# Kernel tuning notes

Hardware: AMD Instinct MI355X
Metric: run time of the kernel (lower is better)

## Reference

```python
import jax, jax.numpy as jnp
import numpy as np

B, N, F_IN, H, FO = 4, 2048, 256, 4, 64


def setup_inputs() -> dict:
    key = jax.random.key(0)
    k1, k2, k3, k4, k5 = jax.random.split(key, 5)
    x = jax.random.normal(k1, (B, N, F_IN), dtype=jnp.float32)
    # random 0/1 adjacency with self-loops so every row of softmax is finite
    adj = jax.random.randint(k2, (N, N), 0, 2).astype(jnp.float32)
    adj = jnp.maximum(adj, jnp.eye(N, dtype=jnp.float32))
    # parameters (xavier-uniform style)
    lim_w = float(np.sqrt(6.0 / (F_IN + H * FO)))
    W = jax.random.uniform(k3, (F_IN, H * FO), minval=-lim_w, maxval=lim_w, dtype=jnp.float32)
    lim_a = float(np.sqrt(6.0 / (H + FO)))
    a_src = jax.random.uniform(k4, (H, FO), minval=-lim_a, maxval=lim_a, dtype=jnp.float32)
    a_dst = jax.random.uniform(k5, (H, FO), minval=-lim_a, maxval=lim_a, dtype=jnp.float32)
    return {"x": x, "adj": adj, "W": W, "a_src": a_src, "a_dst": a_dst}


def reference(x, adj, W, a_src, a_dst):
    # h: (B, N, H, FO)
    h = (x @ W).reshape(B, N, H, FO)
    attn_src = jnp.einsum("bnhf,hf->bnh", h, a_src)  # (B,N,H)
    attn_dst = jnp.einsum("bnhf,hf->bnh", h, a_dst)  # (B,N,H)
    # scores[b,i,j,h] = src[b,i,h] + dst[b,j,h]
    scores = attn_src[:, :, None, :] + attn_dst[:, None, :, :]
    scores = jax.nn.leaky_relu(scores, negative_slope=0.2)
    mask = (adj == 0)[None, :, :, None]  # (1,N,N,1)
    scores = jnp.where(mask, -jnp.inf, scores)
    attn = jax.nn.softmax(scores, axis=2)  # softmax over neighbors j
    # dropout is identity in eval mode / p=0
    out = jnp.einsum("bijh,bjhf->bihf", attn, h)  # (B,N,H,FO)
    return out.reshape(B, N, H * FO)  # concat=True
```

## Files before the change

### kernel.cpp

```cpp
#include <hip/hip_runtime.h>
#include <hip/hip_bf16.h>
#include <math.h>

#define B 4
#define N 2048
#define FIN 256
#define H 4
#define FO 64
#define M (B*N)
#define HF (H*FO)

typedef __attribute__((ext_vector_type(8))) short short8;
typedef __attribute__((ext_vector_type(4))) float float4v;
typedef __attribute__((ext_vector_type(4))) int int4v;

#if __has_builtin(__builtin_amdgcn_exp2f)
#define EXP2(x) __builtin_amdgcn_exp2f(x)
#else
#define EXP2(x) exp2f(x)
#endif

static __device__ __forceinline__ unsigned int pk_rne(float a, float b) {
  unsigned int ua = __builtin_bit_cast(unsigned int, a);
  unsigned int ub = __builtin_bit_cast(unsigned int, b);
  ua += 0x7fffu + ((ua >> 16) & 1u);
  ub += 0x7fffu + ((ub >> 16) & 1u);
  return (ua >> 16) | (ub & 0xffff0000u);
}

static __device__ __forceinline__ unsigned int pk_trunc(float a, float b) {
#if __has_builtin(__builtin_amdgcn_perm)
  return __builtin_amdgcn_perm(__builtin_bit_cast(unsigned int, b),
                               __builtin_bit_cast(unsigned int, a), 0x07060302u);
#else
  return (__builtin_bit_cast(unsigned int, a) >> 16) |
         (__builtin_bit_cast(unsigned int, b) & 0xffff0000u);
#endif
}

static __device__ __forceinline__ void split_pair(float x0, float x1,
                                                  unsigned int& hi, unsigned int& lo) {
  unsigned int u0 = __builtin_bit_cast(unsigned int, x0);
  unsigned int u1 = __builtin_bit_cast(unsigned int, x1);
  hi = (u0 >> 16) | (u1 & 0xffff0000u);
  float h0 = __builtin_bit_cast(float, u0 & 0xffff0000u);
  float h1 = __builtin_bit_cast(float, u1 & 0xffff0000u);
  unsigned int l0 = __builtin_bit_cast(unsigned int, x0 - h0);
  unsigned int l1 = __builtin_bit_cast(unsigned int, x1 - h1);
  lo = (l0 >> 16) | (l1 & 0xffff0000u);
}

static __device__ __forceinline__ unsigned int fenc(float f) {
  unsigned int b = __builtin_bit_cast(unsigned int, f);
  return (b & 0x80000000u) ? ~b : (b | 0x80000000u);
}
static __device__ __forceinline__ float fdec(unsigned int e) {
  unsigned int b = (e & 0x80000000u) ? (e & 0x7fffffffu) : ~e;
  return __builtin_bit_cast(float, b);
}

__global__ __launch_bounds__(256) void prep_wx(const float* __restrict__ Wsrc,
                                               const float* __restrict__ X,
                                               unsigned short* __restrict__ Wf_hi,
                                               unsigned short* __restrict__ Wf_lo,
                                               unsigned short* __restrict__ Xf_hi,
                                               unsigned short* __restrict__ Xf_lo,
                                               unsigned int* __restrict__ DmaxEnc) {
  const int blk = blockIdx.x;
  const int t = threadIdx.x;
  __shared__ float lds[64][65];
  if (blk < 16) {
    if (blk == 0 && t < 16) DmaxEnc[t] = 0u;
    const int k0 = (blk >> 2) * 64;
    const int h  = blk & 3;
    const int n0 = h * 64;
    const int c4 = (t & 15) * 4;
    #pragma unroll
    for (int rep = 0; rep < 4; ++rep) {
      const int kl = (t >> 4) + 16 * rep;
      const float4 v = *(const float4*)(Wsrc + (size_t)(k0 + kl) * HF + n0 + c4);
      lds[kl][c4 + 0] = v.x; lds[kl][c4 + 1] = v.y;
      lds[kl][c4 + 2] = v.z; lds[kl][c4 + 3] = v.w;
    }
    __syncthreads();
    #pragma unroll
    for (int rep = 0; rep < 2; ++rep) {
      const int s   = t + rep * 256;
      const int kcl = s >> 8;
      const int tt  = (s >> 6) & 3;
      const int ln  = s & 63;
      const int fL  = tt * 16 + (ln & 15);
      const int kb  = kcl * 32 + (ln >> 4) * 8;
      unsigned int hv[4], lv[4];
      #pragma unroll
      for (int p = 0; p < 4; ++p)
        split_pair(lds[kb + 2 * p][fL], lds[kb + 2 * p + 1][fL], hv[p], lv[p]);
      const size_t off = ((((size_t)h * 8 + (k0 >> 5) + kcl) * 4 + tt) << 9) + ln * 8;
      *(uint4*)(Wf_hi + off) = make_uint4(hv[0], hv[1], hv[2], hv[3]);
      *(uint4*)(Wf_lo + off) = make_uint4(lv[0], lv[1], lv[2], lv[3]);
    }
    return;
  }
  const int xblk  = blk - 16;
  const int mrow0 = xblk * 64;
  for (int ktile = 0; ktile < 4; ++ktile) {
    if (ktile) __syncthreads();
    const int k0 = ktile * 64;
    const int c4 = (t & 15) * 4;
    #pragma unroll
    for (int rep = 0; rep < 4; ++rep) {
      const int rl = (t >> 4) + 16 * rep;
      const float4 v = *(const float4*)(X + (size_t)(mrow0 + rl) * FIN + k0 + c4);
      lds[rl][c4 + 0] = v.x; lds[rl][c4 + 1] = v.y;
      lds[rl][c4 + 2] = v.z; lds[rl][c4 + 3] = v.w;
    }
    __syncthreads();
    #pragma unroll
    for (int rep = 0; rep < 2; ++rep) {
      const int s   = t + rep * 256;
      const int mt  = s >> 7;
      const int kcl = (s >> 6) & 1;
      const int ln  = s & 63;
      const int mrl = mt * 16 + (ln & 15);
      const int kb  = kcl * 32 + (ln >> 4) * 8;
      unsigned int hv[4], lv[4];
      #pragma unroll
      for (int p = 0; p < 4; ++p)
        split_pair(lds[mrl][kb + 2 * p], lds[mrl][kb + 2 * p + 1], hv[p], lv[p]);
      const size_t off = (((size_t)(xblk * 4 + mt) * 8 + (ktile * 2 + kcl)) << 9) + ln * 8;
      *(uint4*)(Xf_hi + off) = make_uint4(hv[0], hv[1], hv[2], hv[3]);
      *(uint4*)(Xf_lo + off) = make_uint4(lv[0], lv[1], lv[2], lv[3]);
    }
  }
}

__global__ __launch_bounds__(256) void gemm_fused(const unsigned short* __restrict__ Xf_hi,
                                                  const unsigned short* __restrict__ Xf_lo,
                                                  const unsigned short* __restrict__ Wf_hi,
                                                  const unsigned short* __restrict__ Wf_lo,
                                                  const float* __restrict__ adj,
                                                  const float* __restrict__ a_src,
                                                  const float* __restrict__ a_dst,
                                                  float* __restrict__ Srcv,
                                                  float2* __restrict__ Epair,
                                                  unsigned int* __restrict__ DmaxEnc,
                                                  unsigned long long* __restrict__ packed,
                                                  unsigned short* __restrict__ Hf) {
  if (blockIdx.x >= 512) {
    const int row = blockIdx.x - 512;
    const int pw = threadIdx.x >> 6, pl = threadIdx.x & 63;
    const float* ar = adj + (size_t)row * N;
    for (int c = pw; c < N / 64; c += 4) {
      unsigned long long m = __ballot(ar[c * 64 + pl] != 0.f);
      if (pl == 0) packed[(size_t)row * (N / 64) + c] = m;
    }
    return;
  }
  __shared__ unsigned short sh[64][72];
  __shared__ float smax[4];
  const int xcd  = blockIdx.x & 7;
  const int slot = blockIdx.x >> 3;
  const int mb = xcd * 16 + (slot >> 2);
  const int h  = slot & 3;
  const int w = threadIdx.x >> 6, lane = threadIdx.x & 63;
  const int fl = lane & 15, quad = lane >> 4;
  const float L2E = 1.4426950408889634f;

  const float4v zero = {0.f, 0.f, 0.f, 0.f};
  float4v acc[4] = {zero, zero, zero, zero};

  const size_t abase = (((size_t)(mb * 4 + w) * 8) << 9) + lane * 8;
  #pragma unroll
  for (int kc = 0; kc < 8; ++kc) {
    const short8 Ahi = *(const short8*)(Xf_hi + abase + ((size_t)kc << 9));
    const short8 Alo = *(const short8*)(Xf_lo + abase + ((size_t)kc << 9));
    #pragma unroll
    for (int t = 0; t < 4; ++t) {
      const size_t woff = ((((size_t)h * 8 + kc) * 4 + t) << 9) + lane * 8;
      const short8 Bhi = *(const short8*)(Wf_hi + woff);
      const short8 Blo = *(const short8*)(Wf_lo + woff);
      acc[t] = __builtin_amdgcn_mfma_f32_16x16x32_bf16(Ahi, Bhi, acc[t], 0, 0, 0);
      acc[t] = __builtin_amdgcn_mfma_f32_16x16x32_bf16(Alo, Bhi, acc[t], 0, 0, 0);
      acc[t] = __builtin_amdgcn_mfma_f32_16x16x32_bf16(Ahi, Blo, acc[t], 0, 0, 0);
    }
  }

  const int bb  = (mb * 64) >> 11;
  const int n0w = (mb * 64) & (N - 1);
  const int bh  = bb * H + h;
  float as[4], ad[4];
  #pragma unroll
  for (int t = 0; t < 4; ++t) {
    as[t] = a_src[h * FO + t * 16 + fl];
    ad[t] = a_dst[h * FO + t * 16 + fl];
  }
  float wmax = -INFINITY;
  #pragma unroll
  for (int reg = 0; reg < 4; ++reg) {
    float sv = 0.f, dv = 0.f;
    #pragma unroll
    for (int t = 0; t < 4; ++t) {
      sv = fmaf(acc[t][reg], as[t], sv);
      dv = fmaf(acc[t][reg], ad[t], dv);
    }
    #pragma unroll
    for (int off = 1; off <= 8; off <<= 1) {
      sv += __shfl_xor(sv, off, 64);
      dv += __shfl_xor(dv, off, 64);
    }
    wmax = fmaxf(wmax, dv);
    if (fl == 0) {
      const int node = n0w + w * 16 + quad * 4 + reg;
      Srcv[(bh << 11) + node] = sv;
      float2 e;
      e.x = EXP2(dv * L2E);
      e.y = EXP2(dv * (0.2f * L2E));
      Epair[(bh << 11) + node] = e;
    }
  }
  wmax = fmaxf(wmax, __shfl_xor(wmax, 16, 64));
  wmax = fmaxf(wmax, __shfl_xor(wmax, 32, 64));
  if (lane == 0) smax[w] = wmax;

  #pragma unroll
  for (int t = 0; t < 4; ++t) {
    const int nl = w * 16 + quad * 4;
    *(unsigned int*)&sh[t * 16 + fl][nl]     = pk_rne(acc[t][0], acc[t][1]);
    *(unsigned int*)&sh[t * 16 + fl][nl + 2] = pk_rne(acc[t][2], acc[t][3]);
  }
  __syncthreads();
  if (threadIdx.x == 0) {
    const float bmax = fmaxf(fmaxf(smax[0], smax[1]), fmaxf(smax[2], smax[3]));
    atomicMax(DmaxEnc + bh, fenc(bmax));
  }
  const int jc0 = n0w >> 5;
  #pragma unroll
  for (int rep = 0; rep < 2; ++rep) {
    const int s = (int)threadIdx.x + rep * 256;
    const int jcl = s >> 8;
    const int tt  = (s >> 6) & 3;
    const int ln  = s & 63;
    const int f    = tt * 16 + (ln & 15);
    const int node = jcl * 32 + (ln >> 4) * 8;
    unsigned short* dsth = Hf + (((size_t)bh * 64 + jc0 + jcl) * 4 + tt) * 512 + ln * 8;
    *(uint4*)dsth = *(const uint4*)&sh[f][node];
  }
}

__global__ __launch_bounds__(512) void gat_mfma(const unsigned char* __restrict__ pb,
                                                const float* __restrict__ Src,
                                                const float2* __restrict__ Epair,
                                                const unsigned int* __restrict__ DmaxEnc,
                                                const unsigned short* __restrict__ Hf,
                                                float* __restrict__ out) {
  const int xcd  = blockIdx.x & 7;
  const int slot = blockIdx.x >> 3;
  const int b    = xcd >> 1;
  const int i0   = ((xcd & 1) * 32 + slot) * 32;
  const int w    = threadIdx.x >> 6;
  const int lane = threadIdx.x & 63;
  const int h    = w & 3;
  const int jh   = w >> 2;
  const int bh   = b * H + h;
  const int fl   = lane & 15;
  const int kk   = (lane >> 4) * 8;
  const float L2E = 1.4426950408889634f;

  const int row0 = i0 + fl;
  const int row1 = i0 + 16 + fl;
  const float dmx = fdec(DmaxEnc[bh]);
  const float s0 = Src[(bh << 11) + row0];
  const float s1 = Src[(bh << 11) + row1];
  const float u0 = s0 + dmx, m0 = fmaxf(u0, 0.2f * u0);
  const float u1 = s1 + dmx, m1 = fmaxf(u1, 0.2f * u1);
  const float c1a = EXP2((s0 - m0) * L2E), c2a = EXP2((0.2f * s0 - m0) * L2E);
  const float c1b = EXP2((s1 - m1) * L2E), c2b = EXP2((0.2f * s1 - m1) * L2E);
  const float ta = EXP2(-s0 * L2E), tb = EXP2(-s1 * L2E);
  const float* ep = (const float*)(Epair + (bh << 11));
  const unsigned char* pb0 = pb + (size_t)row0 * (N / 8);
  const unsigned char* pb1 = pb + (size_t)row1 * (N / 8);
  const unsigned short* hfb = Hf + (size_t)bh * 64 * 2048 + lane * 8;

  const short onebf = 0x3F80;
  short8 ones;
  #pragma unroll
  for (int jj = 0; jj < 8; ++jj) ones[jj] = onebf;

  const float4v zero = {0.f, 0.f, 0.f, 0.f};
  float4v acc[2][4];
  float4v accL[2];
  #pragma unroll
  for (int rt = 0; rt < 2; ++rt) {
    accL[rt] = zero;
    #pragma unroll
    for (int t = 0; t < 4; ++t) acc[rt][t] = zero;
  }

  const int jbeg = jh * (N / 2);
  short8 nb0, nb1, nb2, nb3;
  float4 nq0, nq1, nq2, nq3;
  unsigned int nm0, nm1;
  {
    const unsigned short* hc = hfb + (size_t)(jbeg >> 5) * 2048;
    nb0 = *(const short8*)(hc + 0 * 512);
    nb1 = *(const short8*)(hc + 1 * 512);
    nb2 = *(const short8*)(hc + 2 * 512);
    nb3 = *(const short8*)(hc + 3 * 512);
    nq0 = *(const float4*)(ep + 2 * (jbeg + kk) + 0);
    nq1 = *(const float4*)(ep + 2 * (jbeg + kk) + 4);
    nq2 = *(const float4*)(ep + 2 * (jbeg + kk) + 8);
    nq3 = *(const float4*)(ep + 2 * (jbeg + kk) + 12);
    nm0 = pb0[(jbeg + kk) >> 3];
    nm1 = pb1[(jbeg + kk) >> 3];
  }

  for (int it = 0; it < 32; ++it) {
    const short8 b0 = nb0, b1 = nb1, b2 = nb2, b3 = nb3;
    const float4 q0 = nq0, q1 = nq1, q2 = nq2, q3 = nq3;
    const unsigned int mk0 = nm0, mk1 = nm1;
    if (it < 31) {
      const int jn = jbeg + (it + 1) * 32;
      const unsigned short* hc = hfb + (size_t)(jn >> 5) * 2048;
      nb0 = *(const short8*)(hc + 0 * 512);
      nb1 = *(const short8*)(hc + 1 * 512);
      nb2 = *(const short8*)(hc + 2 * 512);
      nb3 = *(const short8*)(hc + 3 * 512);
      nq0 = *(const float4*)(ep + 2 * (jn + kk) + 0);
      nq1 = *(const float4*)(ep + 2 * (jn + kk) + 4);
      nq2 = *(const float4*)(ep + 2 * (jn + kk) + 8);
      nq3 = *(const float4*)(ep + 2 * (jn + kk) + 12);
      nm0 = pb0[(jn + kk) >> 3];
      nm1 = pb1[(jn + kk) >> 3];
    }
    const float E1v[8] = {q0.x, q0.z, q1.x, q1.z, q2.x, q2.z, q3.x, q3.z};
    const float E2v[8] = {q0.y, q0.w, q1.y, q1.w, q2.y, q2.w, q3.y, q3.w};
    int p0i[4], p1i[4];
    #pragma unroll
    for (int p = 0; p < 4; ++p) {
      const int e0 = 2 * p, e1 = 2 * p + 1;
      const bool sa0 = E1v[e0] > ta;
      float va0 = (sa0 ? c1a : c2a) * (sa0 ? E1v[e0] : E2v[e0]);
      va0 = ((mk0 >> e0) & 1u) ? va0 : 0.f;
      const bool sa1 = E1v[e1] > ta;
      float va1 = (sa1 ? c1a : c2a) * (sa1 ? E1v[e1] : E2v[e1]);
      va1 = ((mk0 >> e1) & 1u) ? va1 : 0.f;
      p0i[p] = (int)pk_trunc(va0, va1);
      const bool sb0 = E1v[e0] > tb;
      float vb0 = (sb0 ? c1b : c2b) * (sb0 ? E1v[e0] : E2v[e0]);
      vb0 = ((mk1 >> e0) & 1u) ? vb0 : 0.f;
      const bool sb1 = E1v[e1] > tb;
      float vb1 = (sb1 ? c1b : c2b) * (sb1 ? E1v[e1] : E2v[e1]);
      vb1 = ((mk1 >> e1) & 1u) ? vb1 : 0.f;
      p1i[p] = (int)pk_trunc(vb0, vb1);
    }
    const short8 p0 = __builtin_bit_cast(short8, (int4v){p0i[0], p0i[1], p0i[2], p0i[3]});
    const short8 p1 = __builtin_bit_cast(short8, (int4v){p1i[0], p1i[1], p1i[2], p1i[3]});
    acc[0][0] = __builtin_amdgcn_mfma_f32_16x16x32_bf16(p0, b0, acc[0][0], 0, 0, 0);
    acc[0][1] = __builtin_amdgcn_mfma_f32_16x16x32_bf16(p0, b1, acc[0][1], 0, 0, 0);
    acc[0][2] = __builtin_amdgcn_mfma_f32_16x16x32_bf16(p0, b2, acc[0][2], 0, 0, 0);
    acc[0][3] = __builtin_amdgcn_mfma_f32_16x16x32_bf16(p0, b3, acc[0][3], 0, 0, 0);
    accL[0]   = __builtin_amdgcn_mfma_f32_16x16x32_bf16(p0, ones, accL[0], 0, 0, 0);
    acc[1][0] = __builtin_amdgcn_mfma_f32_16x16x32_bf16(p1, b0, acc[1][0], 0, 0, 0);
    acc[1][1] = __builtin_amdgcn_mfma_f32_16x16x32_bf16(p1, b1, acc[1][1], 0, 0, 0);
    acc[1][2] = __builtin_amdgcn_mfma_f32_16x16x32_bf16(p1, b2, acc[1][2], 0, 0, 0);
    acc[1][3] = __builtin_amdgcn_mfma_f32_16x16x32_bf16(p1, b3, acc[1][3], 0, 0, 0);
    accL[1]   = __builtin_amdgcn_mfma_f32_16x16x32_bf16(p1, ones, accL[1], 0, 0, 0);
  }

  __shared__ float4v parts[4][64][11];
  if (jh == 1) {
    #pragma unroll
    for (int rt = 0; rt < 2; ++rt) {
      #pragma unroll
      for (int t = 0; t < 4; ++t) parts[h][lane][rt * 5 + t] = acc[rt][t];
      parts[h][lane][rt * 5 + 4] = accL[rt];
    }
  }
  __syncthreads();
  if (jh == 0) {
    #pragma unroll
    for (int rt = 0; rt < 2; ++rt) {
      #pragma unroll
      for (int t = 0; t < 4; ++t) acc[rt][t] += parts[h][lane][rt * 5 + t];
      accL[rt] += parts[h][lane][rt * 5 + 4];
    }
    const int quad = lane >> 4;
    #pragma unroll
    for (int rt = 0; rt < 2; ++rt) {
      #pragma unroll
      for (int reg = 0; reg < 4; ++reg) {
        const int r = i0 + rt * 16 + quad * 4 + reg;
        const float invl = 1.f / accL[rt][reg];
        float* op = out + ((size_t)(b * N) + r) * HF + h * FO + fl;
        #pragma unroll
        for (int t = 0; t < 4; ++t) op[t * 16] = acc[rt][t][reg] * invl;
      }
    }
  }
}

extern "C" void kernel_launch(void* const* d_in, const int* in_sizes, int n_in,
                              void* d_out, int out_size, void* d_ws, size_t ws_size,
                              hipStream_t stream) {
  const float* x     = (const float*)d_in[0];
  const float* adj   = (const float*)d_in[1];
  const float* W     = (const float*)d_in[2];
  const float* a_src = (const float*)d_in[3];
  const float* a_dst = (const float*)d_in[4];
  float* out = (float*)d_out;

  char* p = (char*)d_ws;
  float* Srcv = (float*)p;                 p += (size_t)B * H * N * 4;
  float2* Epair = (float2*)p;              p += (size_t)B * H * N * 8;
  unsigned int* DmaxEnc = (unsigned int*)p; p += 256;
  unsigned short* Wfh = (unsigned short*)p; p += (size_t)HF * FIN * 2;
  unsigned short* Wfl = (unsigned short*)p; p += (size_t)HF * FIN * 2;
  unsigned short* Xfh = (unsigned short*)p; p += (size_t)M * FIN * 2;
  unsigned short* Xfl = (unsigned short*)p; p += (size_t)M * FIN * 2;
  unsigned short* Hf  = (unsigned short*)p; p += (size_t)M * HF * 2;
  unsigned long long* packed = (unsigned long long*)p;

  prep_wx<<<dim3(144), dim3(256), 0, stream>>>(W, x, Wfh, Wfl, Xfh, Xfl, DmaxEnc);
  gemm_fused<<<dim3(512 + N), dim3(256), 0, stream>>>(Xfh, Xfl, Wfh, Wfl, adj,
                                                      a_src, a_dst,
                                                      Srcv, Epair, DmaxEnc,
                                                      packed, Hf);
  gat_mfma<<<dim3(B * (N / 32)), dim3(512), 0, stream>>>((const unsigned char*)packed,
                                                         Srcv, Epair, DmaxEnc, Hf, out);
}
```

Baseline: 128.3 us.

## Switch attention aggregation to fp16 MFMA with packed-half weight computation

Stores the projected features H and the exp factors E1/E2 as fp16 instead of bf16/fp32 pairs. The weight computation becomes packed-half max of two products, replacing the threshold compare and select, and masking uses sign-extended bit masks. The aggregation uses f16 MFMA. Separately, the X-conversion prep kernel is split across four times as many blocks, one per k-tile, to raise parallelism. This cuts VALU work and load bytes in the inner loop, but fp16 range and precision may cause overflow or accuracy loss in the exp factors.

Result: faster. 121.9 us (-5.0%).

```diff
diff --git a/kernel.cpp b/kernel.cpp
--- a/kernel.cpp
+++ b/kernel.cpp
@@ -11,6 +11,8 @@
 #define HF (H*FO)
 
 typedef __attribute__((ext_vector_type(8))) short short8;
+typedef __attribute__((ext_vector_type(8))) _Float16 half8;
+typedef __attribute__((ext_vector_type(2))) _Float16 half2v;
 typedef __attribute__((ext_vector_type(4))) float float4v;
 typedef __attribute__((ext_vector_type(4))) int int4v;
 
@@ -19,24 +21,6 @@
 #else
 #define EXP2(x) exp2f(x)
 #endif
-
-static __device__ __forceinline__ unsigned int pk_rne(float a, float b) {
-  unsigned int ua = __builtin_bit_cast(unsigned int, a);
-  unsigned int ub = __builtin_bit_cast(unsigned int, b);
-  ua += 0x7fffu + ((ua >> 16) & 1u);
-  ub += 0x7fffu + ((ub >> 16) & 1u);
-  return (ua >> 16) | (ub & 0xffff0000u);
-}
-
-static __device__ __forceinline__ unsigned int pk_trunc(float a, float b) {
-#if __has_builtin(__builtin_amdgcn_perm)
-  return __builtin_amdgcn_perm(__builtin_bit_cast(unsigned int, b),
-                               __builtin_bit_cast(unsigned int, a), 0x07060302u);
-#else
-  return (__builtin_bit_cast(unsigned int, a) >> 16) |
-         (__builtin_bit_cast(unsigned int, b) & 0xffff0000u);
-#endif
-}
 
 static __device__ __forceinline__ void split_pair(float x0, float x1,
                                                   unsigned int& hi, unsigned int& lo) {
@@ -57,6 +41,21 @@
 static __device__ __forceinline__ float fdec(unsigned int e) {
   unsigned int b = (e & 0x80000000u) ? (e & 0x7fffffffu) : ~e;
   return __builtin_bit_cast(float, b);
+}
+
+static __device__ __forceinline__ unsigned int bit_sext(unsigned int v, int k) {
+#if __has_builtin(__builtin_amdgcn_sbfe)
+  return (unsigned int)__builtin_amdgcn_sbfe((int)v, k, 1);
+#else
+  return (unsigned int)(((int)(v << (31 - k))) >> 31);
+#endif
+}
+static __device__ __forceinline__ unsigned int pm2(unsigned int mk, int p) {
+  return __builtin_amdgcn_perm(bit_sext(mk, 2 * p + 1), bit_sext(mk, 2 * p), 0x07060302u);
+}
+static __device__ __forceinline__ unsigned int f16pk(float a, float b) {
+  auto h = __builtin_amdgcn_cvt_pkrtz(a, b);
+  return __builtin_bit_cast(unsigned int, h);
 }
 
 __global__ __launch_bounds__(256) void prep_wx(const float* __restrict__ Wsrc,
@@ -101,36 +100,35 @@
     }
     return;
   }
-  const int xblk  = blk - 16;
+  const int xb2   = blk - 16;
+  const int xblk  = xb2 >> 2;
+  const int ktile = xb2 & 3;
   const int mrow0 = xblk * 64;
-  for (int ktile = 0; ktile < 4; ++ktile) {
-    if (ktile) __syncthreads();
-    const int k0 = ktile * 64;
-    const int c4 = (t & 15) * 4;
-    #pragma unroll
-    for (int rep = 0; rep < 4; ++rep) {
-      const int rl = (t >> 4) + 16 * rep;
-      const float4 v = *(const float4*)(X + (size_t)(mrow0 + rl) * FIN + k0 + c4);
-      lds[rl][c4 + 0] = v.x; lds[rl][c4 + 1] = v.y;
-      lds[rl][c4 + 2] = v.z; lds[rl][c4 + 3] = v.w;
-    }
-    __syncthreads();
-    #pragma unroll
-    for (int rep = 0; rep < 2; ++rep) {
-      const int s   = t + rep * 256;
-      const int mt  = s >> 7;
-      const int kcl = (s >> 6) & 1;
-      const int ln  = s & 63;
-      const int mrl = mt * 16 + (ln & 15);
-      const int kb  = kcl * 32 + (ln >> 4) * 8;
-      unsigned int hv[4], lv[4];
-      #pragma unroll
-      for (int p = 0; p < 4; ++p)
-        split_pair(lds[mrl][kb + 2 * p], lds[mrl][kb + 2 * p + 1], hv[p], lv[p]);
-      const size_t off = (((size_t)(xblk * 4 + mt) * 8 + (ktile * 2 + kcl)) << 9) + ln * 8;
-      *(uint4*)(Xf_hi + off) = make_uint4(hv[0], hv[1], hv[2], hv[3]);
-      *(uint4*)(Xf_lo + off) = make_uint4(lv[0], lv[1], lv[2], lv[3]);
-    }
+  const int k0 = ktile * 64;
+  const int c4 = (t & 15) * 4;
+  #pragma unroll
+  for (int rep = 0; rep < 4; ++rep) {
+    const int rl = (t >> 4) + 16 * rep;
+    const float4 v = *(const float4*)(X + (size_t)(mrow0 + rl) * FIN + k0 + c4);
+    lds[rl][c4 + 0] = v.x; lds[rl][c4 + 1] = v.y;
+    lds[rl][c4 + 2] = v.z; lds[rl][c4 + 3] = v.w;
+  }
+  __syncthreads();
+  #pragma unroll
+  for (int rep = 0; rep < 2; ++rep) {
+    const int s   = t + rep * 256;
+    const int mt  = s >> 7;
+    const int kcl = (s >> 6) & 1;
+    const int ln  = s & 63;
+    const int mrl = mt * 16 + (ln & 15);
+    const int kb  = kcl * 32 + (ln >> 4) * 8;
+    unsigned int hv[4], lv[4];
+    #pragma unroll
+    for (int p = 0; p < 4; ++p)
+      split_pair(lds[mrl][kb + 2 * p], lds[mrl][kb + 2 * p + 1], hv[p], lv[p]);
+    const size_t off = (((size_t)(xblk * 4 + mt) * 8 + (ktile * 2 + kcl)) << 9) + ln * 8;
+    *(uint4*)(Xf_hi + off) = make_uint4(hv[0], hv[1], hv[2], hv[3]);
+    *(uint4*)(Xf_lo + off) = make_uint4(lv[0], lv[1], lv[2], lv[3]);
   }
 }
 
@@ -142,7 +140,8 @@
                                                   const float* __restrict__ a_src,
                                                   const float* __restrict__ a_dst,
                                                   float* __restrict__ Srcv,
-                                                  float2* __restrict__ Epair,
+                                                  unsigned short* __restrict__ E1h,
+                                                  unsigned short* __restrict__ E2h,
                                                   unsigned int* __restrict__ DmaxEnc,
                                                   unsigned long long* __restrict__ packed,
                                                   unsigned short* __restrict__ Hf) {
@@ -212,10 +211,10 @@
     if (fl == 0) {
       const int node = n0w + w * 16 + quad * 4 + reg;
       Srcv[(bh << 11) + node] = sv;
-      float2 e;
-      e.x = EXP2(dv * L2E);
-      e.y = EXP2(dv * (0.2f * L2E));
-      Epair[(bh << 11) + node] = e;
+      const unsigned int eu = f16pk(EXP2(dv * L2E),
+                                    EXP2(dv * (0.2f * L2E)));
+      E1h[(bh << 11) + node] = (unsigned short)(eu & 0xffffu);
+      E2h[(bh << 11) + node] = (unsigned short)(eu >> 16);
     }
   }
   wmax = fmaxf(wmax, __shfl_xor(wmax, 16, 64));
@@ -225,8 +224,8 @@
   #pragma unroll
   for (int t = 0; t < 4; ++t) {
     const int nl = w * 16 + quad * 4;
-    *(unsigned int*)&sh[t * 16 + fl][nl]     = pk_rne(acc[t][0], acc[t][1]);
-    *(unsigned int*)&sh[t * 16 + fl][nl + 2] = pk_rne(acc[t][2], acc[t][3]);
+    *(unsigned int*)&sh[t * 16 + fl][nl]     = f16pk(acc[t][0], acc[t][1]);
+    *(unsigned int*)&sh[t * 16 + fl][nl + 2] = f16pk(acc[t][2], acc[t][3]);
   }
   __syncthreads();
   if (threadIdx.x == 0) {
@@ -249,7 +248,8 @@
 
 __global__ __launch_bounds__(512) void gat_mfma(const unsigned char* __restrict__ pb,
                                                 const float* __restrict__ Src,
-                                                const float2* __restrict__ Epair,
+                                                const unsigned short* __restrict__ E1h,
+                                                const unsigned short* __restrict__ E2h,
                                                 const unsigned int* __restrict__ DmaxEnc,
                                                 const unsigned short* __restrict__ Hf,
                                                 float* __restrict__ out) {
@@ -275,16 +275,19 @@
   const float u1 = s1 + dmx, m1 = fmaxf(u1, 0.2f * u1);
   const float c1a = EXP2((s0 - m0) * L2E), c2a = EXP2((0.2f * s0 - m0) * L2E);
   const float c1b = EXP2((s1 - m1) * L2E), c2b = EXP2((0.2f * s1 - m1) * L2E);
-  const float ta = EXP2(-s0 * L2E), tb = EXP2(-s1 * L2E);
-  const float* ep = (const float*)(Epair + (bh << 11));
+  const half2v c1a2 = {(_Float16)c1a, (_Float16)c1a};
+  const half2v c2a2 = {(_Float16)c2a, (_Float16)c2a};
+  const half2v c1b2 = {(_Float16)c1b, (_Float16)c1b};
+  const half2v c2b2 = {(_Float16)c2b, (_Float16)c2b};
   const unsigned char* pb0 = pb + (size_t)row0 * (N / 8);
   const unsigned char* pb1 = pb + (size_t)row1 * (N / 8);
   const unsigned short* hfb = Hf + (size_t)bh * 64 * 2048 + lane * 8;
-
-  const short onebf = 0x3F80;
-  short8 ones;
-  #pragma unroll
-  for (int jj = 0; jj < 8; ++jj) ones[jj] = onebf;
+  const unsigned short* e1b = E1h + (bh << 11);
+  const unsigned short* e2b = E2h + (bh << 11);
+
+  half8 ones;
+  #pragma unroll
+  for (int jj = 0; jj < 8; ++jj) ones[jj] = (_Float16)1.0f;
 
   const float4v zero = {0.f, 0.f, 0.f, 0.f};
   float4v acc[2][4];
@@ -298,7 +301,7 @@
 
   const int jbeg = jh * (N / 2);
   short8 nb0, nb1, nb2, nb3;
-  float4 nq0, nq1, nq2, nq3;
+  uint4 nE1, nE2;
   unsigned int nm0, nm1;
   {
     const unsigned short* hc = hfb + (size_t)(jbeg >> 5) * 2048;
@@ -306,17 +309,15 @@
     nb1 = *(const short8*)(hc + 1 * 512);
     nb2 = *(const short8*)(hc + 2 * 512);
     nb3 = *(const short8*)(hc + 3 * 512);
-    nq0 = *(const float4*)(ep + 2 * (jbeg + kk) + 0);
-    nq1 = *(const float4*)(ep + 2 * (jbeg + kk) + 4);
-    nq2 = *(const float4*)(ep + 2 * (jbeg + kk) + 8);
-    nq3 = *(const float4*)(ep + 2 * (jbeg + kk) + 12);
+    nE1 = *(const uint4*)(e1b + jbeg + kk);
+    nE2 = *(const uint4*)(e2b + jbeg + kk);
     nm0 = pb0[(jbeg + kk) >> 3];
     nm1 = pb1[(jbeg + kk) >> 3];
   }
 
   for (int it = 0; it < 32; ++it) {
     const short8 b0 = nb0, b1 = nb1, b2 = nb2, b3 = nb3;
-    const float4 q0 = nq0, q1 = nq1, q2 = nq2, q3 = nq3;
+    const uint4 E1q = nE1, E2q = nE2;
     const unsigned int mk0 = nm0, mk1 = nm1;
     if (it < 31) {
       const int jn = jbeg + (it + 1) * 32;
@@ -325,46 +326,39 @@
       nb1 = *(const short8*)(hc + 1 * 512);
       nb2 = *(const short8*)(hc + 2 * 512);
       nb3 = *(const short8*)(hc + 3 * 512);
-      nq0 = *(const float4*)(ep + 2 * (jn + kk) + 0);
-      nq1 = *(const float4*)(ep + 2 * (jn + kk) + 4);
-      nq2 = *(const float4*)(ep + 2 * (jn + kk) + 8);
-      nq3 = *(const float4*)(ep + 2 * (jn + kk) + 12);
+      nE1 = *(const uint4*)(e1b + jn + kk);
+      nE2 = *(const uint4*)(e2b + jn + kk);
       nm0 = pb0[(jn + kk) >> 3];
       nm1 = pb1[(jn + kk) >> 3];
     }
-    const float E1v[8] = {q0.x, q0.z, q1.x, q1.z, q2.x, q2.z, q3.x, q3.z};
-    const float E2v[8] = {q0.y, q0.w, q1.y, q1.w, q2.y, q2.w, q3.y, q3.w};
+    const unsigned int e1w[4] = {E1q.x, E1q.y, E1q.z, E1q.w};
+    const unsigned int e2w[4] = {E2q.x, E2q.y, E2q.z, E2q.w};
     int p0i[4], p1i[4];
     #pragma unroll
     for (int p = 0; p < 4; ++p) {
-      const int e0 = 2 * p, e1 = 2 * p + 1;
-      const bool sa0 = E1v[e0] > ta;
-      float va0 = (sa0 ? c1a : c2a) * (sa0 ? E1v[e0] : E2v[e0]);
-      va0 = ((mk0 >> e0) & 1u) ? va0 : 0.f;
-      const bool sa1 = E1v[e1] > ta;
-      float va1 = (sa1 ? c1a : c2a) * (sa1 ? E1v[e1] : E2v[e1]);
-      va1 = ((mk0 >> e1) & 1u) ? va1 : 0.f;
-      p0i[p] = (int)pk_trunc(va0, va1);
-      const bool sb0 = E1v[e0] > tb;
-      float vb0 = (sb0 ? c1b : c2b) * (sb0 ? E1v[e0] : E2v[e0]);
-      vb0 = ((mk1 >> e0) & 1u) ? vb0 : 0.f;
-      const bool sb1 = E1v[e1] > tb;
-      float vb1 = (sb1 ? c1b : c2b) * (sb1 ? E1v[e1] : E2v[e1]);
-      vb1 = ((mk1 >> e1) & 1u) ? vb1 : 0.f;
-      p1i[p] = (int)pk_trunc(vb0, vb1);
-    }
-    const short8 p0 = __builtin_bit_cast(short8, (int4v){p0i[0], p0i[1], p0i[2], p0i[3]});
-    const short8 p1 = __builtin_bit_cast(short8, (int4v){p1i[0], p1i[1], p1i[2], p1i[3]});
-    acc[0][0] = __builtin_amdgcn_mfma_f32_16x16x32_bf16(p0, b0, acc[0][0], 0, 0, 0);
-    acc[0][1] = __builtin_amdgcn_mfma_f32_16x16x32_bf16(p0, b1, acc[0][1], 0, 0, 0);
-    acc[0][2] = __builtin_amdgcn_mfma_f32_16x16x32_bf16(p0, b2, acc[0][2], 0, 0, 0);
-    acc[0][3] = __builtin_amdgcn_mfma_f32_16x16x32_bf16(p0, b3, acc[0][3], 0, 0, 0);
-    accL[0]   = __builtin_amdgcn_mfma_f32_16x16x32_bf16(p0, ones, accL[0], 0, 0, 0);
-    acc[1][0] = __builtin_amdgcn_mfma_f32_16x16x32_bf16(p1, b0, acc[1][0], 0, 0, 0);
-    acc[1][1] = __builtin_amdgcn_mfma_f32_16x16x32_bf16(p1, b1, acc[1][1], 0, 0, 0);
-    acc[1][2] = __builtin_amdgcn_mfma_f32_16x16x32_bf16(p1, b2, acc[1][2], 0, 0, 0);
-    acc[1][3] = __builtin_amdgcn_mfma_f32_16x16x32_bf16(p1, b3, acc[1][3], 0, 0, 0);
-    accL[1]   = __builtin_amdgcn_mfma_f32_16x16x32_bf16(p1, ones, accL[1], 0, 0, 0);
+      const half2v e1 = __builtin_bit_cast(half2v, e1w[p]);
+      const half2v e2 = __builtin_bit_cast(half2v, e2w[p]);
+      const half2v wa = __builtin_elementwise_max(c1a2 * e1, c2a2 * e2);
+      const half2v wb = __builtin_elementwise_max(c1b2 * e1, c2b2 * e2);
+      p0i[p] = (int)(__builtin_bit_cast(unsigned int, wa) & pm2(mk0, p));
+      p1i[p] = (int)(__builtin_bit_cast(unsigned int, wb) & pm2(mk1, p));
+    }
+    const half8 p0 = __builtin_bit_cast(half8, (int4v){p0i[0], p0i[1], p0i[2], p0i[3]});
+    const half8 p1 = __builtin_bit_cast(half8, (int4v){p1i[0], p1i[1], p1i[2], p1i[3]});
+    const half8 hb0 = __builtin_bit_cast(half8, b0);
+    const half8 hb1 = __builtin_bit_cast(half8, b1);
+    const half8 hb2 = __builtin_bit_cast(half8, b2);
+    const half8 hb3 = __builtin_bit_cast(half8, b3);
+    acc[0][0] = __builtin_amdgcn_mfma_f32_16x16x32_f16(p0, hb0, acc[0][0], 0, 0, 0);
+    acc[0][1] = __builtin_amdgcn_mfma_f32_16x16x32_f16(p0, hb1, acc[0][1], 0, 0, 0);
+    acc[0][2] = __builtin_amdgcn_mfma_f32_16x16x32_f16(p0, hb2, acc[0][2], 0, 0, 0);
+    acc[0][3] = __builtin_amdgcn_mfma_f32_16x16x32_f16(p0, hb3, acc[0][3], 0, 0, 0);
+    accL[0]   = __builtin_amdgcn_mfma_f32_16x16x32_f16(p0, ones, accL[0], 0, 0, 0);
+    acc[1][0] = __builtin_amdgcn_mfma_f32_16x16x32_f16(p1, hb0, acc[1][0], 0, 0, 0);
+    acc[1][1] = __builtin_amdgcn_mfma_f32_16x16x32_f16(p1, hb1, acc[1][1], 0, 0, 0);
+    acc[1][2] = __builtin_amdgcn_mfma_f32_16x16x32_f16(p1, hb2, acc[1][2], 0, 0, 0);
+    acc[1][3] = __builtin_amdgcn_mfma_f32_16x16x32_f16(p1, hb3, acc[1][3], 0, 0, 0);
+    accL[1]   = __builtin_amdgcn_mfma_f32_16x16x32_f16(p1, ones, accL[1], 0, 0, 0);
   }
 
   __shared__ float4v parts[4][64][11];
@@ -410,8 +404,9 @@
   float* out = (float*)d_out;
 
   char* p = (char*)d_ws;
-  float* Srcv = (float*)p;                 p += (size_t)B * H * N * 4;
-  float2* Epair = (float2*)p;              p += (size_t)B * H * N * 8;
+  float* Srcv = (float*)p;                  p += (size_t)B * H * N * 4;
+  unsigned short* E1h = (unsigned short*)p; p += (size_t)B * H * N * 2;
+  unsigned short* E2h = (unsigned short*)p; p += (size_t)B * H * N * 2;
   unsigned int* DmaxEnc = (unsigned int*)p; p += 256;
   unsigned short* Wfh = (unsigned short*)p; p += (size_t)HF * FIN * 2;
   unsigned short* Wfl = (unsigned short*)p; p += (size_t)HF * FIN * 2;
@@ -420,11 +415,11 @@
   unsigned short* Hf  = (unsigned short*)p; p += (size_t)M * HF * 2;
   unsigned long long* packed = (unsigned long long*)p;
 
-  prep_wx<<<dim3(144), dim3(256), 0, stream>>>(W, x, Wfh, Wfl, Xfh, Xfl, DmaxEnc);
+  prep_wx<<<dim3(528), dim3(256), 0, stream>>>(W, x, Wfh, Wfl, Xfh, Xfl, DmaxEnc);
   gemm_fused<<<dim3(512 + N), dim3(256), 0, stream>>>(Xfh, Xfl, Wfh, Wfl, adj,
                                                       a_src, a_dst,
-                                                      Srcv, Epair, DmaxEnc,
+                                                      Srcv, E1h, E2h, DmaxEnc,
                                                       packed, Hf);
   gat_mfma<<<dim3(B * (N / 32)), dim3(512), 0, stream>>>((const unsigned char*)packed,
-                                                         Srcv, Epair, DmaxEnc, Hf, out);
-}
+                                                         Srcv, E1h, E2h, DmaxEnc, Hf, out);
+}
```
